# Performance work log

Hardware: AMD Instinct MI355X
Metric: run time of the kernel (lower is better)

## Reference

```python
import jax, jax.numpy as jnp
import numpy as np

INPUT_DIM = 1024
HIDDEN_DIM = 64  # per-head dim
NUM_HEADS = 16
LN_EPS = 1e-5


def setup_inputs() -> dict:
    key = jax.random.key(0)
    ks = jax.random.split(key, 12)
    B, S, D = 2, 2048, INPUT_DIM
    HD = HIDDEN_DIM * NUM_HEADS
    s_in = 1.0 / np.sqrt(D)
    s_hd = 1.0 / np.sqrt(HD)
    return {
        "x": jax.random.normal(ks[0], (B, S, D), dtype=jnp.float32),
        "Wq": jax.random.normal(ks[1], (D, HD), dtype=jnp.float32) * s_in,
        "bq": jax.random.normal(ks[2], (HD,), dtype=jnp.float32) * 0.02,
        "Wk": jax.random.normal(ks[3], (D, HD), dtype=jnp.float32) * s_in,
        "bk": jax.random.normal(ks[4], (HD,), dtype=jnp.float32) * 0.02,
        "Wv": jax.random.normal(ks[5], (D, HD), dtype=jnp.float32) * s_in,
        "bv": jax.random.normal(ks[6], (HD,), dtype=jnp.float32) * 0.02,
        "Wo": jax.random.normal(ks[7], (HD, D), dtype=jnp.float32) * s_hd,
        "bo": jax.random.normal(ks[8], (D,), dtype=jnp.float32) * 0.02,
        "gamma": jnp.ones((D,), dtype=jnp.float32),
        "beta": jnp.zeros((D,), dtype=jnp.float32),
    }


def _layer_norm(y, gamma, beta):
    mu = jnp.mean(y, axis=-1, keepdims=True)
    var = jnp.mean(jnp.square(y - mu), axis=-1, keepdims=True)
    return (y - mu) * jax.lax.rsqrt(var + LN_EPS) * gamma + beta


def reference(x, Wq, bq, Wk, bk, Wv, bv, Wo, bo, gamma, beta):
    B, S, D = x.shape
    H, Hd = NUM_HEADS, HIDDEN_DIM
    # Faithful to the torch module: (B,S,H*Hd) -> reshape (B,H,S,Hd) WITHOUT transpose.
    Q = (x @ Wq + bq).reshape(B, H, S, Hd)
    K = (x @ Wk + bk).reshape(B, H, S, Hd)
    V = (x @ Wv + bv).reshape(B, H, S, Hd)
    scores = jnp.einsum("bhqd,bhkd->bhqk", Q, K) / jnp.sqrt(jnp.float32(Hd))
    attn = jax.nn.softmax(scores, axis=-1)  # dropout=0 -> identity
    ctx = jnp.einsum("bhqk,bhkd->bhqd", attn, V).reshape(B, S, H * Hd)
    out = _layer_norm(x + (ctx @ Wo + bo), gamma, beta)
    return jax.nn.gelu(out, approximate=False)
```

## Files before the change

### kernel.cpp

```cpp
#include <hip/hip_runtime.h>
#include <hip/hip_bf16.h>
#include <cstdint>
#include <cstddef>


#define SEQ   2048
#define DIM   1024
#define NHEAD 16
#define HDIM  64
#define ROWS  4096

#define QSCALE 0.1803368801111204f

typedef __attribute__((ext_vector_type(8))) __bf16 bf16x8;
typedef __attribute__((ext_vector_type(4))) float floatx4;
typedef __attribute__((ext_vector_type(8))) unsigned short ushortx8;

__device__ __forceinline__ unsigned short f2bf(float f) {
  unsigned int u = __float_as_uint(f);
  u += 0x7FFFu + ((u >> 16) & 1u);
  return (unsigned short)(u >> 16);
}

__device__ __forceinline__ unsigned int pk2bf(float a, float b) {
  float2 f; f.x = a; f.y = b;
  __hip_bfloat162 h = __float22bfloat162_rn(f);
  return *(unsigned int*)&h;
}

__device__ __forceinline__ void glds16(const unsigned short* g,
                                       unsigned short* l) {
  __builtin_amdgcn_global_load_lds(
      (const __attribute__((address_space(1))) void*)g,
      (__attribute__((address_space(3))) void*)l, 16, 0, 0);
}

__global__ __launch_bounds__(256) void cvt_bf16(const float* __restrict__ in,
                                                unsigned short* __restrict__ out,
                                                int n4) {
  int i = blockIdx.x * 256 + threadIdx.x;
  if (i >= n4) return;
  float4 v = ((const float4*)in)[i];
  ushort4 o;
  o.x = f2bf(v.x); o.y = f2bf(v.y); o.z = f2bf(v.z); o.w = f2bf(v.w);
  ((ushort4*)out)[i] = o;
}

__global__ __launch_bounds__(256) void transpose_w4(
    const float* __restrict__ Wq, const float* __restrict__ Wk,
    const float* __restrict__ Wv, const float* __restrict__ Wo,
    unsigned short* __restrict__ Wqkvt, unsigned short* __restrict__ Wot) {
  __shared__ float t[32][33];
  const int z = blockIdx.z;
  const float* in = (z == 0) ? Wq : (z == 1) ? Wk : (z == 2) ? Wv : Wo;
  unsigned short* out = (z < 3) ? Wqkvt + (size_t)z * DIM * DIM : Wot;
  const int bx = blockIdx.x * 32, by = blockIdx.y * 32;
  const int tx = threadIdx.x, ty = threadIdx.y;
#pragma unroll
  for (int i = ty; i < 32; i += 8)
    t[i][tx] = in[(size_t)(by + i) * DIM + bx + tx];
  __syncthreads();
#pragma unroll
  for (int i = ty; i < 32; i += 8)
    out[(size_t)(bx + i) * DIM + by + tx] = f2bf(t[tx][i]);
}

__global__ __launch_bounds__(256) void transpose_v(
    const unsigned short* __restrict__ Vb,
    unsigned short* __restrict__ VbT) {
  __shared__ unsigned short t[64][65];
  const int bh = blockIdx.y;
  const int s0 = blockIdx.x * 64;
  const int tx = threadIdx.x;
  const int ty = threadIdx.y;
  const unsigned short* src = Vb + (size_t)bh * (SEQ * HDIM);
  unsigned short* dst = VbT + (size_t)bh * (SEQ * HDIM);
#pragma unroll
  for (int i = ty; i < 64; i += 4)
    t[i][tx] = src[(size_t)(s0 + i) * HDIM + tx];
  __syncthreads();
#pragma unroll
  for (int i = ty; i < 64; i += 4)
    dst[(size_t)i * SEQ + s0 + tx] = t[tx][i];
}

__global__ __launch_bounds__(256, 3) void gemm_qkv(
    const unsigned short* __restrict__ A,
    const unsigned short* __restrict__ Wt,
    const float* __restrict__ bq, const float* __restrict__ bk,
    const float* __restrict__ bv,
    unsigned short* __restrict__ Qb, unsigned short* __restrict__ Kb,
    unsigned short* __restrict__ Vb) {
  constexpr int K = DIM;
  __shared__ unsigned short As[128 * 64];
  __shared__ unsigned short Bs[128 * 64];
  const int tid  = threadIdx.x;
  const int lane = tid & 63, wave = tid >> 6;
  const int l16  = lane & 15, quad = lane >> 4;
  const int wm   = (wave & 1) * 64, wn = (wave >> 1) * 64;
  const int tm   = blockIdx.y * 128, tn = blockIdx.x * 128;
  const int grow = lane >> 3, gcol = (lane & 7) * 8;

  floatx4 acc[4][4] = {};

  for (int k0 = 0; k0 < K; k0 += 64) {
    __syncthreads();
#pragma unroll
    for (int p = 0; p < 4; ++p) {
      const int q = wave * 4 + p;
      const int row = q * 8 + grow;
      glds16(&A [(size_t)(tm + row) * K + k0 + gcol], &As[q * 512]);
      glds16(&Wt[(size_t)(tn + row) * K + k0 + gcol], &Bs[q * 512]);
    }
    __syncthreads();
#pragma unroll
    for (int step = 0; step < 2; ++step) {
      const int kk = step * 32 + quad * 8;
      bf16x8 af[4], bfr[4];
#pragma unroll
      for (int i = 0; i < 4; ++i)
        af[i] = *(const bf16x8*)&As[(wm + i * 16 + l16) * 64 + kk];
#pragma unroll
      for (int j = 0; j < 4; ++j)
        bfr[j] = *(const bf16x8*)&Bs[(wn + j * 16 + l16) * 64 + kk];
#pragma unroll
      for (int i = 0; i < 4; ++i)
#pragma unroll
        for (int j = 0; j < 4; ++j)
          acc[i][j] = __builtin_amdgcn_mfma_f32_16x16x32_bf16(af[i], bfr[j],
                                                              acc[i][j], 0, 0, 0);
    }
  }

#pragma unroll
  for (int j = 0; j < 4; ++j) {
    const int ng  = tn + wn + j * 16 + l16;
    const int seg = ng >> 10;
    const int col = ng & 1023;
    const float* bp    = (seg == 0) ? bq : (seg == 1) ? bk : bv;
    unsigned short* op = (seg == 0) ? Qb : (seg == 1) ? Kb : Vb;
    const float bias = bp[col];
    const float scl  = (seg == 0) ? QSCALE : 1.0f;
#pragma unroll
    for (int i = 0; i < 4; ++i) {
      const int m0 = tm + wm + i * 16 + quad * 4;
#pragma unroll
      for (int r = 0; r < 4; ++r)
        op[(size_t)(m0 + r) * DIM + col] = f2bf((acc[i][j][r] + bias) * scl);
    }
  }
}

__global__ __launch_bounds__(256) void gemm_o(
    const unsigned short* __restrict__ A,
    const unsigned short* __restrict__ Wt,
    const float* __restrict__ bo,
    float* __restrict__ Y) {
  constexpr int K = DIM;
  __shared__ unsigned short As[128 * 64];
  __shared__ unsigned short Bs[64 * 64];
  const int tid  = threadIdx.x;
  const int lane = tid & 63, wave = tid >> 6;
  const int l16  = lane & 15, quad = lane >> 4;
  const int wm   = wave * 32;
  const int tm   = blockIdx.y * 128, tn = blockIdx.x * 64;
  const int grow = lane >> 3, gcol = (lane & 7) * 8;

  floatx4 acc[2][4] = {};

  for (int k0 = 0; k0 < K; k0 += 64) {
    __syncthreads();
#pragma unroll
    for (int p = 0; p < 4; ++p) {
      const int q = wave * 4 + p;
      const int row = q * 8 + grow;
      glds16(&A[(size_t)(tm + row) * K + k0 + gcol], &As[q * 512]);
    }
#pragma unroll
    for (int p = 0; p < 2; ++p) {
      const int q = wave * 2 + p;
      const int row = q * 8 + grow;
      glds16(&Wt[(size_t)(tn + row) * K + k0 + gcol], &Bs[q * 512]);
    }
    __syncthreads();
#pragma unroll
    for (int step = 0; step < 2; ++step) {
      const int kk = step * 32 + quad * 8;
      bf16x8 af[2], bfr[4];
#pragma unroll
      for (int i = 0; i < 2; ++i)
        af[i] = *(const bf16x8*)&As[(wm + i * 16 + l16) * 64 + kk];
#pragma unroll
      for (int j = 0; j < 4; ++j)
        bfr[j] = *(const bf16x8*)&Bs[(j * 16 + l16) * 64 + kk];
#pragma unroll
      for (int i = 0; i < 2; ++i)
#pragma unroll
        for (int j = 0; j < 4; ++j)
          acc[i][j] = __builtin_amdgcn_mfma_f32_16x16x32_bf16(af[i], bfr[j],
                                                              acc[i][j], 0, 0, 0);
    }
  }

#pragma unroll
  for (int j = 0; j < 4; ++j) {
    const int n = tn + j * 16 + l16;
    const float bias = bo[n];
#pragma unroll
    for (int i = 0; i < 2; ++i) {
      const int m0 = tm + wm + i * 16 + quad * 4;
#pragma unroll
      for (int r = 0; r < 4; ++r)
        Y[(size_t)(m0 + r) * DIM + n] = acc[i][j][r] + bias;
    }
  }
}

__global__ __launch_bounds__(128, 2) void attn_fwd(
    const unsigned short* __restrict__ Qb,
    const unsigned short* __restrict__ Kb,
    const unsigned short* __restrict__ VbT,
    unsigned short* __restrict__ ctx) {
  __shared__ unsigned short Kl[64 * 72];
  __shared__ unsigned short Vt[64 * 72];
  __shared__ unsigned short Pl[2][32 * 72];

  const int tid  = threadIdx.x;
  const int lane = tid & 63, wave = tid >> 6;
  const int l16  = lane & 15, quad = lane >> 4;
  const size_t slab = (size_t)blockIdx.y * SEQ * HDIM;
  const unsigned short* Q  = Qb + slab;
  const unsigned short* Kp = Kb + slab;
  const unsigned short* Vp = VbT + slab;
  const int q0 = blockIdx.x * 64 + wave * 32;

  bf16x8 qf[2][2];
#pragma unroll
  for (int h = 0; h < 2; ++h) {
    qf[h][0] = *(const bf16x8*)&Q[(size_t)(q0 + h * 16 + l16) * HDIM + quad * 8];
    qf[h][1] = *(const bf16x8*)&Q[(size_t)(q0 + h * 16 + l16) * HDIM + 32 + quad * 8];
  }

  floatx4 o[2][4] = {};
  float lr[2] = {0.f, 0.f};

  ushortx8 kr[4], vr[4];
#pragma unroll
  for (int p = 0; p < 4; ++p) {
    const int c = p * 128 + tid;
    const int row = c >> 3, col = (c & 7) * 8;
    kr[p] = *(const ushortx8*)&Kp[(size_t)row * HDIM + col];
    vr[p] = *(const ushortx8*)&Vp[((size_t)row << 11) + col];
  }

  for (int kt = 0; kt < SEQ; kt += 64) {
    __syncthreads();
#pragma unroll
    for (int p = 0; p < 4; ++p) {
      const int c = p * 128 + tid;
      const int row = c >> 3, col = (c & 7) * 8;
      *(ushortx8*)&Kl[row * 72 + col] = kr[p];
      *(ushortx8*)&Vt[row * 72 + col] = vr[p];
    }
    __syncthreads();

    if (kt + 64 < SEQ) {
#pragma unroll
      for (int p = 0; p < 4; ++p) {
        const int c = p * 128 + tid;
        const int row = c >> 3, col = (c & 7) * 8;
        kr[p] = *(const ushortx8*)&Kp[(size_t)(kt + 64 + row) * HDIM + col];
        vr[p] = *(const ushortx8*)&Vp[((size_t)row << 11) + kt + 64 + col];
      }
    }

    floatx4 s[2][4] = {};
#pragma unroll
    for (int step = 0; step < 2; ++step) {
      const int kk = step * 32 + quad * 8;
#pragma unroll
      for (int mt = 0; mt < 4; ++mt) {
        bf16x8 kfr = *(const bf16x8*)&Kl[(mt * 16 + l16) * 72 + kk];
        s[0][mt] = __builtin_amdgcn_mfma_f32_16x16x32_bf16(kfr, qf[0][step], s[0][mt], 0, 0, 0);
        s[1][mt] = __builtin_amdgcn_mfma_f32_16x16x32_bf16(kfr, qf[1][step], s[1][mt], 0, 0, 0);
      }
    }

#pragma unroll
    for (int h = 0; h < 2; ++h) {
#pragma unroll
      for (int mt = 0; mt < 4; ++mt) {
        float p0 = __builtin_amdgcn_exp2f(s[h][mt][0]);
        float p1 = __builtin_amdgcn_exp2f(s[h][mt][1]);
        float p2 = __builtin_amdgcn_exp2f(s[h][mt][2]);
        float p3 = __builtin_amdgcn_exp2f(s[h][mt][3]);
        lr[h] += (p0 + p1) + (p2 + p3);
        uint2 pv;
        pv.x = pk2bf(p0, p1);
        pv.y = pk2bf(p2, p3);
        *(uint2*)&Pl[wave][(h * 16 + l16) * 72 + mt * 16 + quad * 4] = pv;
      }
    }
    __asm__ __volatile__("s_waitcnt lgkmcnt(0)" ::: "memory");

#pragma unroll
    for (int step = 0; step < 2; ++step) {
      const int kk = step * 32 + quad * 8;
      bf16x8 pf0 = *(const bf16x8*)&Pl[wave][(l16) * 72 + kk];
      bf16x8 pf1 = *(const bf16x8*)&Pl[wave][(16 + l16) * 72 + kk];
#pragma unroll
      for (int j = 0; j < 4; ++j) {
        bf16x8 vf = *(const bf16x8*)&Vt[(j * 16 + l16) * 72 + kk];
        o[0][j] = __builtin_amdgcn_mfma_f32_16x16x32_bf16(pf0, vf, o[0][j], 0, 0, 0);
        o[1][j] = __builtin_amdgcn_mfma_f32_16x16x32_bf16(pf1, vf, o[1][j], 0, 0, 0);
      }
    }
  }

#pragma unroll
  for (int h = 0; h < 2; ++h) {
    lr[h] += __shfl_xor(lr[h], 16, 64);
    lr[h] += __shfl_xor(lr[h], 32, 64);
  }
  unsigned short* cp = ctx + slab;
#pragma unroll
  for (int h = 0; h < 2; ++h) {
    float lb[4];
#pragma unroll
    for (int r = 0; r < 4; ++r)
      lb[r] = 1.0f / __shfl(lr[h], quad * 4 + r, 64);
#pragma unroll
    for (int j = 0; j < 4; ++j)
#pragma unroll
      for (int r = 0; r < 4; ++r)
        cp[(size_t)(q0 + h * 16 + quad * 4 + r) * HDIM + j * 16 + l16] =
            f2bf(o[h][j][r] * lb[r]);
  }
}

__global__ __launch_bounds__(256) void ln_gelu(
    const float* __restrict__ x, const float* __restrict__ y,
    const float* __restrict__ gamma, const float* __restrict__ beta,
    float* __restrict__ out) {
  const int row = blockIdx.x;
  const int tid = threadIdx.x;
  const float4 xv = ((const float4*)(x + (size_t)row * DIM))[tid];
  const float4 yv = ((const float4*)(y + (size_t)row * DIM))[tid];
  float4 s;
  s.x = xv.x + yv.x; s.y = xv.y + yv.y; s.z = xv.z + yv.z; s.w = xv.w + yv.w;
  float sum = (s.x + s.y) + (s.z + s.w);
  float sq  = (s.x * s.x + s.y * s.y) + (s.z * s.z + s.w * s.w);
#pragma unroll
  for (int off = 1; off < 64; off <<= 1) {
    sum += __shfl_xor(sum, off, 64);
    sq  += __shfl_xor(sq, off, 64);
  }
  __shared__ float red[8];
  const int wave = tid >> 6, lane = tid & 63;
  if (lane == 0) { red[wave] = sum; red[wave + 4] = sq; }
  __syncthreads();
  sum = red[0] + red[1] + red[2] + red[3];
  sq  = red[4] + red[5] + red[6] + red[7];
  const float mu   = sum * (1.0f / DIM);
  const float var  = sq * (1.0f / DIM) - mu * mu;
  const float rstd = rsqrtf(var + 1e-5f);
  const float4 gv = ((const float4*)gamma)[tid];
  const float4 bv = ((const float4*)beta)[tid];
  float4 ov;
  {
    const float v = (s.x - mu) * rstd * gv.x + bv.x;
    ov.x = 0.5f * v * (1.0f + erff(v * 0.70710678118654752f));
  }
  {
    const float v = (s.y - mu) * rstd * gv.y + bv.y;
    ov.y = 0.5f * v * (1.0f + erff(v * 0.70710678118654752f));
  }
  {
    const float v = (s.z - mu) * rstd * gv.z + bv.z;
    ov.z = 0.5f * v * (1.0f + erff(v * 0.70710678118654752f));
  }
  {
    const float v = (s.w - mu) * rstd * gv.w + bv.w;
    ov.w = 0.5f * v * (1.0f + erff(v * 0.70710678118654752f));
  }
  ((float4*)(out + (size_t)row * DIM))[tid] = ov;
}

extern "C" void kernel_launch(void* const* d_in, const int* in_sizes, int n_in,
                              void* d_out, int out_size, void* d_ws, size_t ws_size,
                              hipStream_t stream) {
  (void)in_sizes; (void)n_in; (void)out_size; (void)ws_size;
  const float* x     = (const float*)d_in[0];
  const float* Wq    = (const float*)d_in[1];
  const float* bq    = (const float*)d_in[2];
  const float* Wk    = (const float*)d_in[3];
  const float* bk    = (const float*)d_in[4];
  const float* Wv    = (const float*)d_in[5];
  const float* bv    = (const float*)d_in[6];
  const float* Wo    = (const float*)d_in[7];
  const float* bo    = (const float*)d_in[8];
  const float* gamma = (const float*)d_in[9];
  const float* beta  = (const float*)d_in[10];
  float* out = (float*)d_out;

  char* ws = (char*)d_ws;
  const size_t MB = 1u << 20;
  unsigned short* xb    = (unsigned short*)(ws);
  unsigned short* Wqkvt = (unsigned short*)(ws + 8 * MB);
  unsigned short* Wot   = (unsigned short*)(ws + 14 * MB);
  unsigned short* Qb    = (unsigned short*)(ws + 16 * MB);
  unsigned short* Kb    = (unsigned short*)(ws + 24 * MB);
  unsigned short* VbT   = (unsigned short*)(ws + 32 * MB);
  unsigned short* Vb    = (unsigned short*)(ws + 40 * MB);
  unsigned short* Cx    = (unsigned short*)(ws + 40 * MB);
  float*          Y     = (float*)(ws + 48 * MB);

  cvt_bf16<<<(ROWS * DIM / 4 + 255) / 256, 256, 0, stream>>>(x, xb, ROWS * DIM / 4);
  transpose_w4<<<dim3(32, 32, 4), dim3(32, 8), 0, stream>>>(Wq, Wk, Wv, Wo, Wqkvt, Wot);

  gemm_qkv<<<dim3(24, 32), 256, 0, stream>>>(xb, Wqkvt, bq, bk, bv, Qb, Kb, Vb);
  transpose_v<<<dim3(SEQ / 64, 32), dim3(64, 4), 0, stream>>>(Vb, VbT);
  attn_fwd<<<dim3(32, 32), 128, 0, stream>>>(Qb, Kb, VbT, Cx);
  gemm_o<<<dim3(16, 32), 256, 0, stream>>>(Cx, Wot, bo, Y);
  ln_gelu<<<ROWS, 256, 0, stream>>>(x, Y, gamma, beta, out);
}
```

Before: 228.3 us.

## Pre-swizzle K and V into MFMA fragment order and load directly to registers

Adds a swizzle_kv kernel that rewrites K (in place) and transposed V into per-tile layouts matching the MFMA operand fragment order, so each lane reads its fragments with contiguous 16-byte global loads. The attention kernel drops its shared-memory staging of K/V, the two block barriers per tile, and the register prefetch. It removes the occupancy hint from launch bounds. The cost is an extra kernel launch and a full pass over K and V, and each wave now loads K/V tiles independently from cache with no software prefetch, so global latency may be exposed.

```diff
diff --git a/kernel.cpp b/kernel.cpp
--- a/kernel.cpp
+++ b/kernel.cpp
@@ -82,6 +82,46 @@
 #pragma unroll
   for (int i = ty; i < 64; i += 4)
     dst[(size_t)i * SEQ + s0 + tx] = t[tx][i];
+}
+
+__global__ __launch_bounds__(256) void swizzle_kv(
+    unsigned short* __restrict__ Kb,
+    const unsigned short* __restrict__ VbT,
+    unsigned short* __restrict__ Vs) {
+  __shared__ unsigned short t[64 * 72];
+  const int tile = blockIdx.x;
+  const int bh   = blockIdx.y;
+  const int isV  = blockIdx.z;
+  const int tid  = threadIdx.x;
+  const size_t slab = (size_t)bh * (SEQ * HDIM);
+  if (!isV) {
+    const unsigned short* src = Kb + slab + (size_t)tile * 4096;
+#pragma unroll
+    for (int p = 0; p < 2; ++p) {
+      const int c = p * 256 + tid;
+      const int row = c >> 3, col = (c & 7) * 8;
+      *(ushortx8*)&t[row * 72 + col] = *(const ushortx8*)&src[c * 8];
+    }
+  } else {
+    const unsigned short* src = VbT + slab;
+#pragma unroll
+    for (int p = 0; p < 2; ++p) {
+      const int c = p * 256 + tid;
+      const int row = c >> 3, col = (c & 7) * 8;
+      *(ushortx8*)&t[row * 72 + col] =
+          *(const ushortx8*)&src[(size_t)row * SEQ + tile * 64 + col];
+    }
+  }
+  __syncthreads();
+  unsigned short* dst = (isV ? Vs : Kb) + slab + (size_t)tile * 4096;
+  const int lane = tid & 63, wave = tid >> 6;
+  const int l16 = lane & 15, quad = lane >> 4;
+#pragma unroll
+  for (int f = wave * 2; f < wave * 2 + 2; ++f) {
+    const int step = f >> 2, g = f & 3;
+    *(ushortx8*)&dst[f * 512 + lane * 8] =
+        *(const ushortx8*)&t[(g * 16 + l16) * 72 + step * 32 + quad * 8];
+  }
 }
 
 __global__ __launch_bounds__(256, 3) void gemm_qkv(
@@ -216,13 +256,11 @@
   }
 }
 
-__global__ __launch_bounds__(128, 2) void attn_fwd(
+__global__ __launch_bounds__(128) void attn_fwd(
     const unsigned short* __restrict__ Qb,
-    const unsigned short* __restrict__ Kb,
-    const unsigned short* __restrict__ VbT,
+    const unsigned short* __restrict__ Ks,
+    const unsigned short* __restrict__ Vs,
     unsigned short* __restrict__ ctx) {
-  __shared__ unsigned short Kl[64 * 72];
-  __shared__ unsigned short Vt[64 * 72];
   __shared__ unsigned short Pl[2][32 * 72];
 
   const int tid  = threadIdx.x;
@@ -230,8 +268,8 @@
   const int l16  = lane & 15, quad = lane >> 4;
   const size_t slab = (size_t)blockIdx.y * SEQ * HDIM;
   const unsigned short* Q  = Qb + slab;
-  const unsigned short* Kp = Kb + slab;
-  const unsigned short* Vp = VbT + slab;
+  const unsigned short* Kf = Ks + slab;
+  const unsigned short* Vf = Vs + slab;
   const int q0 = blockIdx.x * 64 + wave * 32;
 
   bf16x8 qf[2][2];
@@ -244,47 +282,26 @@
   floatx4 o[2][4] = {};
   float lr[2] = {0.f, 0.f};
 
-  ushortx8 kr[4], vr[4];
-#pragma unroll
-  for (int p = 0; p < 4; ++p) {
-    const int c = p * 128 + tid;
-    const int row = c >> 3, col = (c & 7) * 8;
-    kr[p] = *(const ushortx8*)&Kp[(size_t)row * HDIM + col];
-    vr[p] = *(const ushortx8*)&Vp[((size_t)row << 11) + col];
-  }
-
-  for (int kt = 0; kt < SEQ; kt += 64) {
-    __syncthreads();
-#pragma unroll
-    for (int p = 0; p < 4; ++p) {
-      const int c = p * 128 + tid;
-      const int row = c >> 3, col = (c & 7) * 8;
-      *(ushortx8*)&Kl[row * 72 + col] = kr[p];
-      *(ushortx8*)&Vt[row * 72 + col] = vr[p];
-    }
-    __syncthreads();
-
-    if (kt + 64 < SEQ) {
-#pragma unroll
-      for (int p = 0; p < 4; ++p) {
-        const int c = p * 128 + tid;
-        const int row = c >> 3, col = (c & 7) * 8;
-        kr[p] = *(const ushortx8*)&Kp[(size_t)(kt + 64 + row) * HDIM + col];
-        vr[p] = *(const ushortx8*)&Vp[((size_t)row << 11) + kt + 64 + col];
+  for (int tile = 0; tile < SEQ / 64; ++tile) {
+    const unsigned short* kb = Kf + (size_t)tile * 4096;
+    const unsigned short* vb = Vf + (size_t)tile * 4096;
+    bf16x8 kf[2][4], vf[2][4];
+#pragma unroll
+    for (int step = 0; step < 2; ++step)
+#pragma unroll
+      for (int g = 0; g < 4; ++g) {
+        kf[step][g] = *(const bf16x8*)&kb[(step * 4 + g) * 512 + lane * 8];
+        vf[step][g] = *(const bf16x8*)&vb[(step * 4 + g) * 512 + lane * 8];
       }
-    }
 
     floatx4 s[2][4] = {};
 #pragma unroll
-    for (int step = 0; step < 2; ++step) {
-      const int kk = step * 32 + quad * 8;
+    for (int step = 0; step < 2; ++step)
 #pragma unroll
       for (int mt = 0; mt < 4; ++mt) {
-        bf16x8 kfr = *(const bf16x8*)&Kl[(mt * 16 + l16) * 72 + kk];
-        s[0][mt] = __builtin_amdgcn_mfma_f32_16x16x32_bf16(kfr, qf[0][step], s[0][mt], 0, 0, 0);
-        s[1][mt] = __builtin_amdgcn_mfma_f32_16x16x32_bf16(kfr, qf[1][step], s[1][mt], 0, 0, 0);
+        s[0][mt] = __builtin_amdgcn_mfma_f32_16x16x32_bf16(kf[step][mt], qf[0][step], s[0][mt], 0, 0, 0);
+        s[1][mt] = __builtin_amdgcn_mfma_f32_16x16x32_bf16(kf[step][mt], qf[1][step], s[1][mt], 0, 0, 0);
       }
-    }
 
 #pragma unroll
     for (int h = 0; h < 2; ++h) {
@@ -310,9 +327,8 @@
       bf16x8 pf1 = *(const bf16x8*)&Pl[wave][(16 + l16) * 72 + kk];
 #pragma unroll
       for (int j = 0; j < 4; ++j) {
-        bf16x8 vf = *(const bf16x8*)&Vt[(j * 16 + l16) * 72 + kk];
-        o[0][j] = __builtin_amdgcn_mfma_f32_16x16x32_bf16(pf0, vf, o[0][j], 0, 0, 0);
-        o[1][j] = __builtin_amdgcn_mfma_f32_16x16x32_bf16(pf1, vf, o[1][j], 0, 0, 0);
+        o[0][j] = __builtin_amdgcn_mfma_f32_16x16x32_bf16(pf0, vf[step][j], o[0][j], 0, 0, 0);
+        o[1][j] = __builtin_amdgcn_mfma_f32_16x16x32_bf16(pf1, vf[step][j], o[1][j], 0, 0, 0);
       }
     }
   }
@@ -411,8 +427,9 @@
   unsigned short* Qb    = (unsigned short*)(ws + 16 * MB);
   unsigned short* Kb    = (unsigned short*)(ws + 24 * MB);
   unsigned short* VbT   = (unsigned short*)(ws + 32 * MB);
+  unsigned short* Cx    = (unsigned short*)(ws + 32 * MB);
   unsigned short* Vb    = (unsigned short*)(ws + 40 * MB);
-  unsigned short* Cx    = (unsigned short*)(ws + 40 * MB);
+  unsigned short* Vs    = (unsigned short*)(ws + 40 * MB);
   float*          Y     = (float*)(ws + 48 * MB);
 
   cvt_bf16<<<(ROWS * DIM / 4 + 255) / 256, 256, 0, stream>>>(x, xb, ROWS * DIM / 4);
@@ -420,7 +437,8 @@
 
   gemm_qkv<<<dim3(24, 32), 256, 0, stream>>>(xb, Wqkvt, bq, bk, bv, Qb, Kb, Vb);
   transpose_v<<<dim3(SEQ / 64, 32), dim3(64, 4), 0, stream>>>(Vb, VbT);
-  attn_fwd<<<dim3(32, 32), 128, 0, stream>>>(Qb, Kb, VbT, Cx);
+  swizzle_kv<<<dim3(SEQ / 64, 32, 2), 256, 0, stream>>>(Kb, VbT, Vs);
+  attn_fwd<<<dim3(32, 32), 128, 0, stream>>>(Qb, Kb, Vs, Cx);
   gemm_o<<<dim3(16, 32), 256, 0, stream>>>(Cx, Wot, bo, Y);
   ln_gelu<<<ROWS, 256, 0, stream>>>(x, Y, gamma, beta, out);
 }
```

New measurement: 227.2 us. Within noise of the previous version (-0.5%).
